# Kernel optimization log

Hardware: AMD Instinct MI355X
Metric: run time of the kernel (lower is better)

Reference implementation:

```python
import jax, jax.numpy as jnp
import numpy as np

X_SIZE = 1024
N_HEADS = 16
N_BASIS = 10
MAX_LEN = 4096
CACHE_KEEP_LEN = 4096
B = 8
T_NEW = 128
T_PREV = 4096
HEAD_DIM = X_SIZE // N_HEADS
LN_EPS = 1e-5


def setup_inputs() -> dict:
    key = jax.random.key(0)
    ks = jax.random.split(key, 9)
    def w(k, shape, s):
        return jax.random.normal(k, shape, dtype=jnp.float32) * s
    inv = 1.0 / np.sqrt(X_SIZE)
    return {
        "X": w(ks[0], (B, T_NEW, X_SIZE), 1.0),
        "cache_K": w(ks[1], (B, T_PREV, X_SIZE), 1.0),
        "cache_V": w(ks[2], (B, T_PREV, X_SIZE), 1.0),
        "Wq": w(ks[3], (X_SIZE, X_SIZE), 0.1 * inv),   # Q_SCALE=0.1 (NormedLinear init scale)
        "bq": jnp.zeros((X_SIZE,), jnp.float32),
        "Wk": w(ks[4], (X_SIZE, X_SIZE), 0.2 * inv),   # K_SCALE=0.2, no bias
        "Wv": w(ks[5], (X_SIZE, X_SIZE), 1.0 * inv),   # V_SCALE*sqrt(scale), no bias
        "Wproj": w(ks[6], (X_SIZE, X_SIZE), 1.0 * inv),
        "bproj": jnp.zeros((X_SIZE,), jnp.float32),
        "Wr": w(ks[7], (X_SIZE, N_BASIS * N_HEADS), 0.1 * inv),  # R_SCALE=0.1
        "br": jnp.zeros((N_BASIS * N_HEADS,), jnp.float32),
        "b_nd": w(ks[8], (N_BASIS, MAX_LEN), 0.2),     # B_SCALE=0.2
        "ln_g": jnp.ones((X_SIZE,), jnp.float32),
        "ln_b": jnp.zeros((X_SIZE,), jnp.float32),
    }


def _split_heads(x, h):
    b, t, e = x.shape
    return x.reshape(b, t, h, e // h).transpose(0, 2, 1, 3).reshape(b * h, t, e // h)


def _merge_heads(x, h):
    bh, t, q = x.shape
    b = bh // h
    return x.reshape(b, h, t, q).transpose(0, 2, 1, 3).reshape(b, t, h * q)


def reference(X, cache_K, cache_V, Wq, bq, Wk, Wv, Wproj, bproj, Wr, br, b_nd, ln_g, ln_b):
    Bsz, t, E = X.shape
    # ln_x
    mu = jnp.mean(X, axis=-1, keepdims=True)
    var = jnp.var(X, axis=-1, keepdims=True)
    Xn = (X - mu) / jnp.sqrt(var + LN_EPS) * ln_g + ln_b
    # projections on new tokens
    Q = Xn @ Wq + bq
    K_new = Xn @ Wk
    V_new = Xn @ Wv
    # update_state: append cache (startfull=max(Tprev-cache_keep_len,0))
    Tprev = cache_K.shape[1]
    start = max(Tprev - CACHE_KEEP_LEN, 0)
    Kf = jnp.concatenate([cache_K[:, start:], K_new], axis=1)  # (B, T, E)
    Vf = jnp.concatenate([cache_V[:, start:], V_new], axis=1)
    T = Kf.shape[1]
    Qh = _split_heads(Q, N_HEADS)   # (B*h, t, q)
    Kh = _split_heads(Kf, N_HEADS)  # (B*h, T, q)
    Vh = _split_heads(Vf, N_HEADS)
    # relattn logits: R_btn (B*h, t, n_basis), bandified basis D_ntT
    R = _split_heads(Xn @ Wr + br, N_HEADS)
    d = (T - t + jnp.arange(t)[:, None]) - jnp.arange(T)[None, :]  # (t, T) time diff
    valid = (d >= 0) & (d < MAX_LEN)
    D = jnp.where(valid[None, :, :], b_nd[:, jnp.clip(d, 0, MAX_LEN - 1)], 0.0)  # (n, t, T)
    extra = jnp.einsum('btn,ntT->btT', R, D)  # (B*h, t, T)
    # causal band bias (mask=None -> default causal mask with maxlen window)
    bias = jnp.where(valid, 0.0, -1e9)[None, :, :]
    logits = bias + extra + jnp.einsum('btq,bTq->btT', Qh, Kh) * (1.0 / np.sqrt(HEAD_DIM))
    W_btT = jax.nn.softmax(logits, axis=-1)
    A = _merge_heads(jnp.einsum('btT,bTq->btq', W_btT, Vh), N_HEADS)  # (B, t, E)
    return X + (A @ Wproj + bproj)
```

## Files before the change

kernel.cpp:

```cpp
#include <hip/hip_runtime.h>
#include <hip/hip_bf16.h>

typedef __bf16 bf16;
typedef __bf16 bf16x8 __attribute__((ext_vector_type(8)));
typedef float f32x4 __attribute__((ext_vector_type(4)));
typedef unsigned short u16;
typedef u16 u16x4 __attribute__((ext_vector_type(4)));

#define MFMA16(a, b, c) __builtin_amdgcn_mfma_f32_16x16x32_bf16(a, b, c, 0, 0, 0)
#define LOG2E 1.44269504f

static __device__ __forceinline__ bf16x8 cvt8(float4 a, float4 b) {
  union { bf16 h[8]; bf16x8 v; } u;
  u.h[0] = (bf16)a.x; u.h[1] = (bf16)a.y; u.h[2] = (bf16)a.z; u.h[3] = (bf16)a.w;
  u.h[4] = (bf16)b.x; u.h[5] = (bf16)b.y; u.h[6] = (bf16)b.z; u.h[7] = (bf16)b.w;
  return u.v;
}

__global__ __launch_bounds__(256) void k_ln(const float* __restrict__ X,
                                            const float* __restrict__ g,
                                            const float* __restrict__ bb,
                                            bf16* __restrict__ Xn) {
  int m = blockIdx.x, t = threadIdx.x;
  const float* row = X + (size_t)m * 1024;
  float4 x = ((const float4*)row)[t];
  float s1 = x.x + x.y + x.z + x.w;
  float s2 = x.x * x.x + x.y * x.y + x.z * x.z + x.w * x.w;
#pragma unroll
  for (int off = 1; off < 64; off <<= 1) {
    s1 += __shfl_xor(s1, off);
    s2 += __shfl_xor(s2, off);
  }
  __shared__ float ws1[4], ws2[4];
  int w = t >> 6;
  if ((t & 63) == 0) { ws1[w] = s1; ws2[w] = s2; }
  __syncthreads();
  s1 = ws1[0] + ws1[1] + ws1[2] + ws1[3];
  s2 = ws2[0] + ws2[1] + ws2[2] + ws2[3];
  float mu = s1 * (1.f / 1024.f);
  float var = s2 * (1.f / 1024.f) - mu * mu;
  float rstd = rsqrtf(var + 1e-5f);
  float4 gg = ((const float4*)g)[t];
  float4 bv = ((const float4*)bb)[t];
  union { bf16 h[4]; u16x4 v; } u;
  u.h[0] = (bf16)((x.x - mu) * rstd * gg.x + bv.x);
  u.h[1] = (bf16)((x.y - mu) * rstd * gg.y + bv.y);
  u.h[2] = (bf16)((x.z - mu) * rstd * gg.z + bv.z);
  u.h[3] = (bf16)((x.w - mu) * rstd * gg.w + bv.w);
  ((u16x4*)(Xn + (size_t)m * 1024))[t] = u.v;
}

__global__ __launch_bounds__(256) void k_convert(const float* __restrict__ Wq,
                                                 const float* __restrict__ Wk,
                                                 const float* __restrict__ Wv,
                                                 const float* __restrict__ Wr,
                                                 const float* __restrict__ Wp,
                                                 bf16* __restrict__ Wt_all,
                                                 bf16* __restrict__ Wpt) {
  __shared__ float tile[64][65];
  int t = threadIdx.x;
  int bn = blockIdx.x / 16, bk = blockIdx.x % 16;
  int n0 = bn * 64, k0 = bk * 64;
#pragma unroll
  for (int it = 0; it < 16; ++it) {
    int idx = t + 256 * it;
    int kl = idx >> 6, nl = idx & 63;
    int n = n0 + nl, k = k0 + kl;
    float v;
    if (n < 1024)       v = Wq[(size_t)k * 1024 + n];
    else if (n < 2048)  v = Wk[(size_t)k * 1024 + (n - 1024)];
    else if (n < 3072)  v = Wv[(size_t)k * 1024 + (n - 2048)];
    else if (n < 3232)  v = Wr[(size_t)k * 160 + (n - 3072)];
    else if (n < 3328)  v = 0.f;
    else                v = Wp[(size_t)k * 1024 + (n - 3328)];
    tile[kl][nl] = v;
  }
  __syncthreads();
#pragma unroll
  for (int it = 0; it < 16; ++it) {
    int idx = t + 256 * it;
    int nl = idx >> 6, kl = idx & 63;
    int n = n0 + nl, k = k0 + kl;
    bf16 v = (bf16)tile[kl][nl];
    if (n < 3328) Wt_all[(size_t)n * 1024 + k] = v;
    else          Wpt[(size_t)(n - 3328) * 1024 + k] = v;
  }
}

template <int MODE>
__global__ __launch_bounds__(256) void k_gemm(const bf16* __restrict__ A,
                                              const bf16* __restrict__ Bw,
                                              bf16* __restrict__ Qb, bf16* __restrict__ Kn,
                                              bf16* __restrict__ Vn, float* __restrict__ Rws,
                                              const float* __restrict__ bq,
                                              const float* __restrict__ br,
                                              float* __restrict__ Out,
                                              const float* __restrict__ bproj,
                                              const float* __restrict__ Xres) {
  __shared__ __align__(16) bf16 As[128][72];
  __shared__ __align__(16) bf16 Bs[128][72];
  int t = threadIdx.x, l = t & 63, wid = t >> 6;
  int ln = l & 15, grp = l >> 4;
  int m0 = blockIdx.y * 128, n0 = blockIdx.x * 128;
  int wr = wid >> 1, wc = wid & 1;
  f32x4 acc[4][4] = {};
  int srow = t >> 1, shalf = (t & 1) * 32;

  for (int kt = 0; kt < 16; ++kt) {
    int k0 = kt * 64;
    const bf16* asrc = A + (size_t)(m0 + srow) * 1024 + k0 + shalf;
    const bf16* bsrc = Bw + (size_t)(n0 + srow) * 1024 + k0 + shalf;
    bf16x8 a0 = ((const bf16x8*)asrc)[0], a1 = ((const bf16x8*)asrc)[1];
    bf16x8 a2 = ((const bf16x8*)asrc)[2], a3 = ((const bf16x8*)asrc)[3];
    bf16x8 b0 = ((const bf16x8*)bsrc)[0], b1 = ((const bf16x8*)bsrc)[1];
    bf16x8 b2 = ((const bf16x8*)bsrc)[2], b3 = ((const bf16x8*)bsrc)[3];
    __syncthreads();
    *(bf16x8*)&As[srow][shalf + 0] = a0;  *(bf16x8*)&As[srow][shalf + 8] = a1;
    *(bf16x8*)&As[srow][shalf + 16] = a2; *(bf16x8*)&As[srow][shalf + 24] = a3;
    *(bf16x8*)&Bs[srow][shalf + 0] = b0;  *(bf16x8*)&Bs[srow][shalf + 8] = b1;
    *(bf16x8*)&Bs[srow][shalf + 16] = b2; *(bf16x8*)&Bs[srow][shalf + 24] = b3;
    __syncthreads();
#pragma unroll
    for (int ks = 0; ks < 2; ++ks) {
      int kk = ks * 32 + grp * 8;
      bf16x8 af[4], bf[4];
#pragma unroll
      for (int is = 0; is < 4; ++is) af[is] = *(const bf16x8*)&As[wr * 64 + is * 16 + ln][kk];
#pragma unroll
      for (int js = 0; js < 4; ++js) bf[js] = *(const bf16x8*)&Bs[wc * 64 + js * 16 + ln][kk];
#pragma unroll
      for (int is = 0; is < 4; ++is)
#pragma unroll
        for (int js = 0; js < 4; ++js) acc[is][js] = MFMA16(af[is], bf[js], acc[is][js]);
    }
  }

#pragma unroll
  for (int is = 0; is < 4; ++is)
#pragma unroll
    for (int js = 0; js < 4; ++js)
#pragma unroll
      for (int r = 0; r < 4; ++r) {
        int m = m0 + wr * 64 + is * 16 + grp * 4 + r;
        int n = n0 + wc * 64 + js * 16 + ln;
        float v = acc[is][js][r];
        if (MODE == 0) {
          int b = m >> 7, il = m & 127;
          if (n < 1024) {
            int h = n >> 6, dm = n & 63;
            Qb[((size_t)(b * 16 + h) * 128 + il) * 64 + dm] = (bf16)((v + bq[n]) * (0.125f * LOG2E));
          } else if (n < 2048) {
            Kn[(size_t)m * 1024 + (n - 1024)] = (bf16)v;
          } else if (n < 3072) {
            Vn[(size_t)m * 1024 + (n - 2048)] = (bf16)v;
          } else if (n < 3232) {
            int e = n - 3072, hh = e / 10, nb = e - hh * 10;
            Rws[((size_t)(b * 16 + hh) * 128 + il) * 10 + nb] = v + br[e];
          }
        } else {
          Out[(size_t)m * 1024 + n] = v + bproj[n] + Xres[(size_t)m * 1024 + n];
        }
      }
}

__global__ __launch_bounds__(512, 4) void k_attn(const float* __restrict__ cacheK,
                                                 const float* __restrict__ cacheV,
                                                 const bf16* __restrict__ Kn,
                                                 const bf16* __restrict__ Vn,
                                                 const bf16* __restrict__ Qb,
                                                 const float* __restrict__ Rws,
                                                 const float* __restrict__ bnd,
                                                 bf16* __restrict__ Opart,
                                                 float* __restrict__ mws,
                                                 float* __restrict__ lws) {
  __shared__ __align__(16) bf16 Ks[2][32][72];
  __shared__ __align__(16) bf16 Vt[2][64][36];
  __shared__ __align__(16) bf16 Gw[8][48][20];
  __shared__ __align__(16) bf16 bTf[516][16];

  int t = threadIdx.x, l = t & 63, w = t >> 6;
  int grp = l >> 4, ln = l & 15;
  int s = blockIdx.x % 12, bh = blockIdx.x / 12;
  int b = bh >> 4, h = bh & 15;
  int jbase = s * 352;
  int dlo0 = 4033 - jbase;

  {
    int q = t;
    int d = dlo0 - 320 + q;
    d = d < 0 ? 0 : (d > 4095 ? 4095 : d);
#pragma unroll
    for (int n = 0; n < 10; ++n) bTf[q][n] = (bf16)bnd[(size_t)n * 4096 + d];
#pragma unroll
    for (int n = 10; n < 16; ++n) bTf[q][n] = (bf16)0.f;
  }
  if (t < 4) {
#pragma unroll
    for (int n = 0; n < 16; ++n) bTf[512 + t][n] = (bf16)0.f;
  }

  int iq = w * 16 + ln;
  bf16x8 qf[2];
  qf[0] = *(const bf16x8*)(Qb + ((size_t)bh * 128 + iq) * 64 + grp * 8);
  qf[1] = *(const bf16x8*)(Qb + ((size_t)bh * 128 + iq) * 64 + 32 + grp * 8);
  bf16x8 rf;
  {
    union { bf16 hh[8]; bf16x8 v; } u;
    const float* rrow = Rws + ((size_t)bh * 128 + iq) * 10;
#pragma unroll
    for (int e = 0; e < 8; ++e) {
      int k = grp * 8 + e;
      u.hh[e] = (bf16)(k < 10 ? rrow[k] * LOG2E : 0.f);
    }
    rf = u.v;
  }

  int krow = t >> 4, kcb = (t & 15) * 4;
  int vjl = t & 31, vd0 = (t >> 5) * 4;
  int vsp = (((vjl >> 2) & 3) << 3) | (((vjl >> 4) & 1) << 2) | (vjl & 3);

  float4 kA, vA;

  auto issue = [&](int jt0) {
    if (jt0 < 4096) {
      kA = *(const float4*)(cacheK + ((size_t)(b * 4096 + jt0 + krow)) * 1024 + h * 64 + kcb);
      vA = *(const float4*)(cacheV + ((size_t)(b * 4096 + jt0 + vjl)) * 1024 + h * 64 + vd0);
    } else {
      u16x4 kN = *(const u16x4*)(Kn + ((size_t)(b * 128 + (jt0 + krow - 4096))) * 1024 + h * 64 + kcb);
      u16x4 vN = *(const u16x4*)(Vn + ((size_t)(b * 128 + (jt0 + vjl - 4096))) * 1024 + h * 64 + vd0);
      union { u16 u; bf16 h; } c;
      c.u = kN[0]; kA.x = (float)c.h; c.u = kN[1]; kA.y = (float)c.h;
      c.u = kN[2]; kA.z = (float)c.h; c.u = kN[3]; kA.w = (float)c.h;
      c.u = vN[0]; vA.x = (float)c.h; c.u = vN[1]; vA.y = (float)c.h;
      c.u = vN[2]; vA.z = (float)c.h; c.u = vN[3]; vA.w = (float)c.h;
    }
  };
  auto stage = [&](int p) {
    union { bf16 hh[4]; u16x4 v; } ku;
    ku.hh[0] = (bf16)kA.x; ku.hh[1] = (bf16)kA.y;
    ku.hh[2] = (bf16)kA.z; ku.hh[3] = (bf16)kA.w;
    *(u16x4*)&Ks[p][krow][kcb] = ku.v;
    Vt[p][vd0 + 0][vsp] = (bf16)vA.x; Vt[p][vd0 + 1][vsp] = (bf16)vA.y;
    Vt[p][vd0 + 2][vsp] = (bf16)vA.z; Vt[p][vd0 + 3][vsp] = (bf16)vA.w;
  };

  issue(jbase);
  stage(0);
  issue(jbase + 32);

  f32x4 Oacc[4] = {};
  float m_r = -1e30f, l_r = 0.f;

  for (int tt = 0; tt < 11; ++tt) {
    int jt0 = jbase + tt * 32;
    int cur = tt & 1;
    __syncthreads();
    if (tt + 1 < 11) stage(cur ^ 1);
    if (tt + 2 < 11) issue(jbase + (tt + 2) * 32);

    __builtin_amdgcn_s_setprio(1);
    f32x4 Sacc[2] = {};
#pragma unroll
    for (int ks = 0; ks < 2; ++ks) {
      int kk = ks * 32 + grp * 8;
#pragma unroll
      for (int js = 0; js < 2; ++js) {
        bf16x8 bfr = *(const bf16x8*)&Ks[cur][js * 16 + ln][kk];
        Sacc[js] = MFMA16(bfr, qf[ks], Sacc[js]);
      }
    }
    int qb = 352 - 32 * tt;
#pragma unroll
    for (int u = 0; u < 3; ++u) {
      bf16x8 bfr = *(const bf16x8*)&bTf[qb + w * 16 + u * 16 + ln][grp * 8];
      f32x4 z = {};
      f32x4 g = MFMA16(rf, bfr, z);
      union { bf16 hh[4]; u16x4 v; } uu;
      uu.hh[0] = (bf16)g[0]; uu.hh[1] = (bf16)g[1];
      uu.hh[2] = (bf16)g[2]; uu.hh[3] = (bf16)g[3];
      *(u16x4*)&Gw[w][u * 16 + ln][grp * 4] = uu.v;
    }
    __builtin_amdgcn_s_setprio(0);

    float mx = -1e30f;
    if (jt0 >= 128 && jt0 < 4066) {
#pragma unroll
      for (int js = 0; js < 2; ++js)
#pragma unroll
        for (int r = 0; r < 4; ++r) {
          int jj = js * 16 + grp * 4 + r;
          int cl = ln - jj + 31;
          float v = Sacc[js][r] + (float)Gw[w][cl][ln];
          Sacc[js][r] = v;
          mx = fmaxf(mx, v);
        }
    } else {
#pragma unroll
      for (int js = 0; js < 2; ++js)
#pragma unroll
        for (int r = 0; r < 4; ++r) {
          int jj = js * 16 + grp * 4 + r;
          int d = 4096 + iq - (jt0 + jj);
          bool valid = ((unsigned)d) < 4096u;
          int cl = ln - jj + 31;
          float g = (float)Gw[w][cl][ln];
          float v = valid ? (Sacc[js][r] + g) : -1e9f;
          Sacc[js][r] = v;
          mx = fmaxf(mx, v);
        }
    }
    mx = fmaxf(mx, __shfl_xor(mx, 16));
    mx = fmaxf(mx, __shfl_xor(mx, 32));

    if (!__all(mx <= m_r + 8.f)) {
      float mnew = fmaxf(m_r, mx);
      float scn = exp2f(m_r - mnew);
      m_r = mnew;
      l_r *= scn;
#pragma unroll
      for (int r = 0; r < 4; ++r) {
        float scr = __shfl(scn, grp * 4 + r, 16);
#pragma unroll
        for (int ds = 0; ds < 4; ++ds) Oacc[ds][r] *= scr;
      }
    }

    union { bf16 hh[8]; bf16x8 v; } p0;
    float rsl = 0.f;
#pragma unroll
    for (int js = 0; js < 2; ++js)
#pragma unroll
      for (int r = 0; r < 4; ++r) {
        float p = exp2f(Sacc[js][r] - m_r);
        rsl += p;
        p0.hh[js * 4 + r] = (bf16)p;
      }
    l_r += rsl;

    __builtin_amdgcn_s_setprio(1);
#pragma unroll
    for (int ds = 0; ds < 4; ++ds) {
      bf16x8 v0 = *(const bf16x8*)&Vt[cur][ds * 16 + ln][grp * 8];
      Oacc[ds] = MFMA16(p0.v, v0, Oacc[ds]);
    }
    __builtin_amdgcn_s_setprio(0);
  }

  l_r += __shfl_xor(l_r, 16);
  l_r += __shfl_xor(l_r, 32);

  int part = s * 128 + bh;
#pragma unroll
  for (int ds = 0; ds < 4; ++ds)
#pragma unroll
    for (int r = 0; r < 4; ++r) {
      int il = w * 16 + grp * 4 + r;
      Opart[((size_t)part * 128 + il) * 64 + ds * 16 + ln] = (bf16)Oacc[ds][r];
    }
  if (grp == 0) {
    mws[(size_t)part * 128 + iq] = m_r;
    lws[(size_t)part * 128 + iq] = l_r;
  }
}

__global__ __launch_bounds__(256) void k_combine(const bf16* __restrict__ Opart,
                                                 const float* __restrict__ mws,
                                                 const float* __restrict__ lws,
                                                 bf16* __restrict__ Aout) {
  __shared__ float msh[12][32], lsh[12][32];
  int bh = blockIdx.x, q = blockIdx.y, t = threadIdx.x;
  int b = bh >> 4, h = bh & 15;
  for (int idx = t; idx < 384; idx += 256) {
    int s = idx >> 5, io = idx & 31;
    msh[s][io] = mws[(size_t)(s * 128 + bh) * 128 + q * 32 + io];
    lsh[s][io] = lws[(size_t)(s * 128 + bh) * 128 + q * 32 + io];
  }
  __syncthreads();
  int dm = t & 63, i4 = t >> 6;
  for (int ii = 0; ii < 8; ++ii) {
    int io = i4 * 8 + ii;
    int i = q * 32 + io;
    float M = -1e30f;
#pragma unroll
    for (int s = 0; s < 12; ++s) M = fmaxf(M, msh[s][io]);
    float L = 0.f, acc = 0.f;
#pragma unroll
    for (int s = 0; s < 12; ++s) {
      float wgt = exp2f(msh[s][io] - M);
      L += wgt * lsh[s][io];
      acc += wgt * (float)Opart[((size_t)(s * 128 + bh) * 128 + i) * 64 + dm];
    }
    Aout[((size_t)(b * 128 + i)) * 1024 + h * 64 + dm] = (bf16)(acc / L);
  }
}

extern "C" void kernel_launch(void* const* d_in, const int* in_sizes, int n_in,
                              void* d_out, int out_size, void* d_ws, size_t ws_size,
                              hipStream_t stream) {
  (void)in_sizes; (void)n_in; (void)out_size; (void)ws_size;
  const float* X      = (const float*)d_in[0];
  const float* cacheK = (const float*)d_in[1];
  const float* cacheV = (const float*)d_in[2];
  const float* Wq     = (const float*)d_in[3];
  const float* bq     = (const float*)d_in[4];
  const float* Wk     = (const float*)d_in[5];
  const float* Wv     = (const float*)d_in[6];
  const float* Wproj  = (const float*)d_in[7];
  const float* bproj  = (const float*)d_in[8];
  const float* Wr     = (const float*)d_in[9];
  const float* br     = (const float*)d_in[10];
  const float* bnd    = (const float*)d_in[11];
  const float* lng    = (const float*)d_in[12];
  const float* lnb    = (const float*)d_in[13];
  float* out = (float*)d_out;

  char* ws = (char*)d_ws;
  bf16* Wt_all = (bf16*)ws;  ws += (size_t)3328 * 1024 * 2;
  bf16* Wpt    = (bf16*)ws;  ws += (size_t)1024 * 1024 * 2;
  bf16* Xn     = (bf16*)ws;  ws += (size_t)1024 * 1024 * 2;
  bf16* Qb     = (bf16*)ws;  ws += (size_t)1024 * 1024 * 2;
  bf16* Kn     = (bf16*)ws;  ws += (size_t)1024 * 1024 * 2;
  bf16* Vn     = (bf16*)ws;  ws += (size_t)1024 * 1024 * 2;
  bf16* Aattn  = (bf16*)ws;  ws += (size_t)1024 * 1024 * 2;
  float* Rws   = (float*)ws; ws += (size_t)128 * 128 * 10 * 4;
  float* mws   = (float*)ws; ws += (size_t)12 * 128 * 128 * 4;
  float* lws   = (float*)ws; ws += (size_t)12 * 128 * 128 * 4;
  bf16* Opart  = (bf16*)ws;  ws += (size_t)12 * 128 * 128 * 64 * 2;

  k_convert<<<dim3(68 * 16), 256, 0, stream>>>(Wq, Wk, Wv, Wr, Wproj, Wt_all, Wpt);
  k_ln<<<dim3(1024), 256, 0, stream>>>(X, lng, lnb, Xn);
  k_gemm<0><<<dim3(26, 8), 256, 0, stream>>>(Xn, Wt_all, Qb, Kn, Vn, Rws, bq, br,
                                             nullptr, nullptr, nullptr);
  k_attn<<<dim3(1536), 512, 0, stream>>>(cacheK, cacheV, Kn, Vn, Qb, Rws, bnd,
                                         Opart, mws, lws);
  k_combine<<<dim3(128, 4), 256, 0, stream>>>(Opart, mws, lws, Aattn);
  k_gemm<1><<<dim3(8, 8), 256, 0, stream>>>(Aattn, Wpt, nullptr, nullptr, nullptr,
                                            nullptr, nullptr, nullptr, out, bproj, X);
}
```

Before: 163.1 us.

## Halve attention block size with two query sub-tiles per wave

Each attention block now runs 4 waves of 256 threads instead of 8 waves of 512, and each wave handles 32 queries as two 16-row sub-tiles. K and V fragments read from LDS are reused across both sub-tiles. Global K/V staging also moves to 8-element loads per thread. The goal is fewer LDS reads and less softmax bookkeeping per MFMA. The cost is more registers and fewer resident waves to hide the latency of the fp32 cache loads.

```diff
diff --git a/kernel.cpp b/kernel.cpp
--- a/kernel.cpp
+++ b/kernel.cpp
@@ -163,7 +163,7 @@
       }
 }
 
-__global__ __launch_bounds__(512, 4) void k_attn(const float* __restrict__ cacheK,
+__global__ __launch_bounds__(256, 3) void k_attn(const float* __restrict__ cacheK,
                                                  const float* __restrict__ cacheV,
                                                  const bf16* __restrict__ Kn,
                                                  const bf16* __restrict__ Vn,
@@ -175,8 +175,8 @@
                                                  float* __restrict__ lws) {
   __shared__ __align__(16) bf16 Ks[2][32][72];
   __shared__ __align__(16) bf16 Vt[2][64][36];
-  __shared__ __align__(16) bf16 Gw[8][48][20];
-  __shared__ __align__(16) bf16 bTf[516][16];
+  __shared__ __align__(16) bf16 Gw[4][64][36];
+  __shared__ __align__(16) bf16 bTf[480][16];
 
   int t = threadIdx.x, l = t & 63, w = t >> 6;
   int grp = l >> 4, ln = l & 15;
@@ -185,71 +185,70 @@
   int jbase = s * 352;
   int dlo0 = 4033 - jbase;
 
-  {
-    int q = t;
-    int d = dlo0 - 320 + q;
+  for (int q = t; q < 480; q += 256) {
+    int d = dlo0 - 288 + q;
     d = d < 0 ? 0 : (d > 4095 ? 4095 : d);
 #pragma unroll
     for (int n = 0; n < 10; ++n) bTf[q][n] = (bf16)bnd[(size_t)n * 4096 + d];
 #pragma unroll
     for (int n = 10; n < 16; ++n) bTf[q][n] = (bf16)0.f;
   }
-  if (t < 4) {
-#pragma unroll
-    for (int n = 0; n < 16; ++n) bTf[512 + t][n] = (bf16)0.f;
-  }
-
-  int iq = w * 16 + ln;
-  bf16x8 qf[2];
-  qf[0] = *(const bf16x8*)(Qb + ((size_t)bh * 128 + iq) * 64 + grp * 8);
-  qf[1] = *(const bf16x8*)(Qb + ((size_t)bh * 128 + iq) * 64 + 32 + grp * 8);
-  bf16x8 rf;
-  {
-    union { bf16 hh[8]; bf16x8 v; } u;
-    const float* rrow = Rws + ((size_t)bh * 128 + iq) * 10;
+
+  int iqb = w * 32 + ln;
+  bf16x8 qf[2][2];
+  bf16x8 rf[2];
+#pragma unroll
+  for (int hh = 0; hh < 2; ++hh) {
+    const bf16* qrow = Qb + ((size_t)bh * 128 + iqb + hh * 16) * 64;
+    qf[hh][0] = *(const bf16x8*)(qrow + grp * 8);
+    qf[hh][1] = *(const bf16x8*)(qrow + 32 + grp * 8);
+    union { bf16 x[8]; bf16x8 v; } u;
+    const float* rrow = Rws + ((size_t)bh * 128 + iqb + hh * 16) * 10;
 #pragma unroll
     for (int e = 0; e < 8; ++e) {
       int k = grp * 8 + e;
-      u.hh[e] = (bf16)(k < 10 ? rrow[k] * LOG2E : 0.f);
-    }
-    rf = u.v;
-  }
-
-  int krow = t >> 4, kcb = (t & 15) * 4;
-  int vjl = t & 31, vd0 = (t >> 5) * 4;
+      u.x[e] = (bf16)(k < 10 ? rrow[k] * LOG2E : 0.f);
+    }
+    rf[hh] = u.v;
+  }
+
+  int krow = t >> 3, kcb = (t & 7) * 8;
+  int vjl = t & 31, vd0 = (t >> 5) * 8;
   int vsp = (((vjl >> 2) & 3) << 3) | (((vjl >> 4) & 1) << 2) | (vjl & 3);
 
-  float4 kA, vA;
+  float4 kA, kB, vA, vB;
 
   auto issue = [&](int jt0) {
     if (jt0 < 4096) {
-      kA = *(const float4*)(cacheK + ((size_t)(b * 4096 + jt0 + krow)) * 1024 + h * 64 + kcb);
-      vA = *(const float4*)(cacheV + ((size_t)(b * 4096 + jt0 + vjl)) * 1024 + h * 64 + vd0);
+      const float* sk = cacheK + ((size_t)(b * 4096 + jt0 + krow)) * 1024 + h * 64 + kcb;
+      kA = *(const float4*)sk;
+      kB = *(const float4*)(sk + 4);
+      const float* sv = cacheV + ((size_t)(b * 4096 + jt0 + vjl)) * 1024 + h * 64 + vd0;
+      vA = *(const float4*)sv;
+      vB = *(const float4*)(sv + 4);
     } else {
-      u16x4 kN = *(const u16x4*)(Kn + ((size_t)(b * 128 + (jt0 + krow - 4096))) * 1024 + h * 64 + kcb);
-      u16x4 vN = *(const u16x4*)(Vn + ((size_t)(b * 128 + (jt0 + vjl - 4096))) * 1024 + h * 64 + vd0);
-      union { u16 u; bf16 h; } c;
-      c.u = kN[0]; kA.x = (float)c.h; c.u = kN[1]; kA.y = (float)c.h;
-      c.u = kN[2]; kA.z = (float)c.h; c.u = kN[3]; kA.w = (float)c.h;
-      c.u = vN[0]; vA.x = (float)c.h; c.u = vN[1]; vA.y = (float)c.h;
-      c.u = vN[2]; vA.z = (float)c.h; c.u = vN[3]; vA.w = (float)c.h;
+      bf16x8 kN = *(const bf16x8*)(Kn + ((size_t)(b * 128 + (jt0 + krow - 4096))) * 1024 + h * 64 + kcb);
+      bf16x8 vN = *(const bf16x8*)(Vn + ((size_t)(b * 128 + (jt0 + vjl - 4096))) * 1024 + h * 64 + vd0);
+      kA = make_float4((float)kN[0], (float)kN[1], (float)kN[2], (float)kN[3]);
+      kB = make_float4((float)kN[4], (float)kN[5], (float)kN[6], (float)kN[7]);
+      vA = make_float4((float)vN[0], (float)vN[1], (float)vN[2], (float)vN[3]);
+      vB = make_float4((float)vN[4], (float)vN[5], (float)vN[6], (float)vN[7]);
     }
   };
   auto stage = [&](int p) {
-    union { bf16 hh[4]; u16x4 v; } ku;
-    ku.hh[0] = (bf16)kA.x; ku.hh[1] = (bf16)kA.y;
-    ku.hh[2] = (bf16)kA.z; ku.hh[3] = (bf16)kA.w;
-    *(u16x4*)&Ks[p][krow][kcb] = ku.v;
+    *(bf16x8*)&Ks[p][krow][kcb] = cvt8(kA, kB);
     Vt[p][vd0 + 0][vsp] = (bf16)vA.x; Vt[p][vd0 + 1][vsp] = (bf16)vA.y;
     Vt[p][vd0 + 2][vsp] = (bf16)vA.z; Vt[p][vd0 + 3][vsp] = (bf16)vA.w;
+    Vt[p][vd0 + 4][vsp] = (bf16)vB.x; Vt[p][vd0 + 5][vsp] = (bf16)vB.y;
+    Vt[p][vd0 + 6][vsp] = (bf16)vB.z; Vt[p][vd0 + 7][vsp] = (bf16)vB.w;
   };
 
   issue(jbase);
   stage(0);
   issue(jbase + 32);
 
-  f32x4 Oacc[4] = {};
-  float m_r = -1e30f, l_r = 0.f;
+  f32x4 Oacc[2][4] = {};
+  float m_r[2] = {-1e30f, -1e30f}, l_r[2] = {0.f, 0.f};
 
   for (int tt = 0; tt < 11; ++tt) {
     int jt0 = jbase + tt * 32;
@@ -258,108 +257,142 @@
     if (tt + 1 < 11) stage(cur ^ 1);
     if (tt + 2 < 11) issue(jbase + (tt + 2) * 32);
 
+    bf16x8 kf[2][2];
+#pragma unroll
+    for (int js = 0; js < 2; ++js)
+#pragma unroll
+      for (int ks = 0; ks < 2; ++ks)
+        kf[js][ks] = *(const bf16x8*)&Ks[cur][js * 16 + ln][ks * 32 + grp * 8];
+
     __builtin_amdgcn_s_setprio(1);
-    f32x4 Sacc[2] = {};
-#pragma unroll
-    for (int ks = 0; ks < 2; ++ks) {
-      int kk = ks * 32 + grp * 8;
-#pragma unroll
-      for (int js = 0; js < 2; ++js) {
-        bf16x8 bfr = *(const bf16x8*)&Ks[cur][js * 16 + ln][kk];
-        Sacc[js] = MFMA16(bfr, qf[ks], Sacc[js]);
+    f32x4 Sacc[2][2] = {};
+#pragma unroll
+    for (int hh = 0; hh < 2; ++hh)
+#pragma unroll
+      for (int ks = 0; ks < 2; ++ks)
+#pragma unroll
+        for (int js = 0; js < 2; ++js)
+          Sacc[hh][js] = MFMA16(kf[js][ks], qf[hh][ks], Sacc[hh][js]);
+
+    int qb = 320 - 32 * tt + w * 32;
+#pragma unroll
+    for (int hh = 0; hh < 2; ++hh)
+#pragma unroll
+      for (int u = 0; u < 3; ++u) {
+        bf16x8 bfr = *(const bf16x8*)&bTf[qb + hh * 16 + u * 16 + ln][grp * 8];
+        f32x4 z = {};
+        f32x4 g = MFMA16(rf[hh], bfr, z);
+        union { bf16 x[4]; u16x4 v; } uu;
+        uu.x[0] = (bf16)g[0]; uu.x[1] = (bf16)g[1];
+        uu.x[2] = (bf16)g[2]; uu.x[3] = (bf16)g[3];
+        *(u16x4*)&Gw[w][hh * 16 + u * 16 + ln][hh * 16 + grp * 4] = uu.v;
       }
-    }
-    int qb = 352 - 32 * tt;
-#pragma unroll
-    for (int u = 0; u < 3; ++u) {
-      bf16x8 bfr = *(const bf16x8*)&bTf[qb + w * 16 + u * 16 + ln][grp * 8];
-      f32x4 z = {};
-      f32x4 g = MFMA16(rf, bfr, z);
-      union { bf16 hh[4]; u16x4 v; } uu;
-      uu.hh[0] = (bf16)g[0]; uu.hh[1] = (bf16)g[1];
-      uu.hh[2] = (bf16)g[2]; uu.hh[3] = (bf16)g[3];
-      *(u16x4*)&Gw[w][u * 16 + ln][grp * 4] = uu.v;
-    }
     __builtin_amdgcn_s_setprio(0);
 
-    float mx = -1e30f;
+    float mx[2] = {-1e30f, -1e30f};
     if (jt0 >= 128 && jt0 < 4066) {
 #pragma unroll
+      for (int hh = 0; hh < 2; ++hh)
+#pragma unroll
+        for (int js = 0; js < 2; ++js)
+#pragma unroll
+          for (int r = 0; r < 4; ++r) {
+            int jj = js * 16 + grp * 4 + r;
+            int cl = hh * 16 + ln - jj + 31;
+            float v = Sacc[hh][js][r] + (float)Gw[w][cl][hh * 16 + ln];
+            Sacc[hh][js][r] = v;
+            mx[hh] = fmaxf(mx[hh], v);
+          }
+    } else {
+#pragma unroll
+      for (int hh = 0; hh < 2; ++hh)
+#pragma unroll
+        for (int js = 0; js < 2; ++js)
+#pragma unroll
+          for (int r = 0; r < 4; ++r) {
+            int jj = js * 16 + grp * 4 + r;
+            int iq = iqb + hh * 16;
+            int d = 4096 + iq - (jt0 + jj);
+            bool valid = ((unsigned)d) < 4096u;
+            int cl = hh * 16 + ln - jj + 31;
+            float g = (float)Gw[w][cl][hh * 16 + ln];
+            float v = valid ? (Sacc[hh][js][r] + g) : -1e9f;
+            Sacc[hh][js][r] = v;
+            mx[hh] = fmaxf(mx[hh], v);
+          }
+    }
+#pragma unroll
+    for (int hh = 0; hh < 2; ++hh) {
+      mx[hh] = fmaxf(mx[hh], __shfl_xor(mx[hh], 16));
+      mx[hh] = fmaxf(mx[hh], __shfl_xor(mx[hh], 32));
+    }
+
+    bool ok = (mx[0] <= m_r[0] + 8.f) && (mx[1] <= m_r[1] + 8.f);
+    if (!__all(ok)) {
+#pragma unroll
+      for (int hh = 0; hh < 2; ++hh) {
+        float mnew = fmaxf(m_r[hh], mx[hh]);
+        float scn = exp2f(m_r[hh] - mnew);
+        m_r[hh] = mnew;
+        l_r[hh] *= scn;
+#pragma unroll
+        for (int r = 0; r < 4; ++r) {
+          float scr = __shfl(scn, grp * 4 + r, 16);
+#pragma unroll
+          for (int ds = 0; ds < 4; ++ds) Oacc[hh][ds][r] *= scr;
+        }
+      }
+    }
+
+    union { bf16 x[8]; bf16x8 v; } p[2];
+#pragma unroll
+    for (int hh = 0; hh < 2; ++hh) {
+      float rsl = 0.f;
+#pragma unroll
       for (int js = 0; js < 2; ++js)
 #pragma unroll
         for (int r = 0; r < 4; ++r) {
-          int jj = js * 16 + grp * 4 + r;
-          int cl = ln - jj + 31;
-          float v = Sacc[js][r] + (float)Gw[w][cl][ln];
-          Sacc[js][r] = v;
-          mx = fmaxf(mx, v);
+          float pv = exp2f(Sacc[hh][js][r] - m_r[hh]);
+          rsl += pv;
+          p[hh].x[js * 4 + r] = (bf16)pv;
         }
-    } else {
-#pragma unroll
-      for (int js = 0; js < 2; ++js)
-#pragma unroll
-        for (int r = 0; r < 4; ++r) {
-          int jj = js * 16 + grp * 4 + r;
-          int d = 4096 + iq - (jt0 + jj);
-          bool valid = ((unsigned)d) < 4096u;
-          int cl = ln - jj + 31;
-          float g = (float)Gw[w][cl][ln];
-          float v = valid ? (Sacc[js][r] + g) : -1e9f;
-          Sacc[js][r] = v;
-          mx = fmaxf(mx, v);
-        }
-    }
-    mx = fmaxf(mx, __shfl_xor(mx, 16));
-    mx = fmaxf(mx, __shfl_xor(mx, 32));
-
-    if (!__all(mx <= m_r + 8.f)) {
-      float mnew = fmaxf(m_r, mx);
-      float scn = exp2f(m_r - mnew);
-      m_r = mnew;
-      l_r *= scn;
+      l_r[hh] += rsl;
+    }
+    bf16x8 vf[4];
+#pragma unroll
+    for (int ds = 0; ds < 4; ++ds) vf[ds] = *(const bf16x8*)&Vt[cur][ds * 16 + ln][grp * 8];
+
+    __builtin_amdgcn_s_setprio(1);
+#pragma unroll
+    for (int hh = 0; hh < 2; ++hh)
+#pragma unroll
+      for (int ds = 0; ds < 4; ++ds)
+        Oacc[hh][ds] = MFMA16(p[hh].v, vf[ds], Oacc[hh][ds]);
+    __builtin_amdgcn_s_setprio(0);
+  }
+
+#pragma unroll
+  for (int hh = 0; hh < 2; ++hh) {
+    l_r[hh] += __shfl_xor(l_r[hh], 16);
+    l_r[hh] += __shfl_xor(l_r[hh], 32);
+  }
+
+  int part = s * 128 + bh;
+#pragma unroll
+  for (int hh = 0; hh < 2; ++hh)
+#pragma unroll
+    for (int ds = 0; ds < 4; ++ds)
 #pragma unroll
       for (int r = 0; r < 4; ++r) {
-        float scr = __shfl(scn, grp * 4 + r, 16);
-#pragma unroll
-        for (int ds = 0; ds < 4; ++ds) Oacc[ds][r] *= scr;
+        int il = w * 32 + hh * 16 + grp * 4 + r;
+        Opart[((size_t)part * 128 + il) * 64 + ds * 16 + ln] = (bf16)Oacc[hh][ds][r];
       }
-    }
-
-    union { bf16 hh[8]; bf16x8 v; } p0;
-    float rsl = 0.f;
-#pragma unroll
-    for (int js = 0; js < 2; ++js)
-#pragma unroll
-      for (int r = 0; r < 4; ++r) {
-        float p = exp2f(Sacc[js][r] - m_r);
-        rsl += p;
-        p0.hh[js * 4 + r] = (bf16)p;
-      }
-    l_r += rsl;
-
-    __builtin_amdgcn_s_setprio(1);
-#pragma unroll
-    for (int ds = 0; ds < 4; ++ds) {
-      bf16x8 v0 = *(const bf16x8*)&Vt[cur][ds * 16 + ln][grp * 8];
-      Oacc[ds] = MFMA16(p0.v, v0, Oacc[ds]);
-    }
-    __builtin_amdgcn_s_setprio(0);
-  }
-
-  l_r += __shfl_xor(l_r, 16);
-  l_r += __shfl_xor(l_r, 32);
-
-  int part = s * 128 + bh;
-#pragma unroll
-  for (int ds = 0; ds < 4; ++ds)
-#pragma unroll
-    for (int r = 0; r < 4; ++r) {
-      int il = w * 16 + grp * 4 + r;
-      Opart[((size_t)part * 128 + il) * 64 + ds * 16 + ln] = (bf16)Oacc[ds][r];
-    }
   if (grp == 0) {
-    mws[(size_t)part * 128 + iq] = m_r;
-    lws[(size_t)part * 128 + iq] = l_r;
+#pragma unroll
+    for (int hh = 0; hh < 2; ++hh) {
+      mws[(size_t)part * 128 + iqb + hh * 16] = m_r[hh];
+      lws[(size_t)part * 128 + iqb + hh * 16] = l_r[hh];
+    }
   }
 }
 
@@ -431,7 +464,7 @@
   k_ln<<<dim3(1024), 256, 0, stream>>>(X, lng, lnb, Xn);
   k_gemm<0><<<dim3(26, 8), 256, 0, stream>>>(Xn, Wt_all, Qb, Kn, Vn, Rws, bq, br,
                                              nullptr, nullptr, nullptr);
-  k_attn<<<dim3(1536), 512, 0, stream>>>(cacheK, cacheV, Kn, Vn, Qb, Rws, bnd,
+  k_attn<<<dim3(1536), 256, 0, stream>>>(cacheK, cacheV, Kn, Vn, Qb, Rws, bnd,
                                          Opart, mws, lws);
   k_combine<<<dim3(128, 4), 256, 0, stream>>>(Opart, mws, lws, Aattn);
   k_gemm<1><<<dim3(8, 8), 256, 0, stream>>>(Aattn, Wpt, nullptr, nullptr, nullptr,
```

Result: slower. 166.8 us (+2.3%).

## Halve attention key splits and restage relative-basis table mid-loop

Applied to the files above, without the earlier changes.

Cuts the split-K count of the attention kernel from 12 to 6, so each block walks 704 keys in 22 tiles instead of 352 in 11. The relative-basis table is restaged halfway through the loop, behind an extra barrier. The table row width also shrinks from 16 to 12 bf16, with fragments read as two 8-byte loads. This halves the partial-output writes and the combine reads, but leaves fewer blocks (768) to fill the GPU and lengthens each block's serial loop.

```diff
diff --git a/kernel.cpp b/kernel.cpp
--- a/kernel.cpp
+++ b/kernel.cpp
@@ -176,28 +176,30 @@
   __shared__ __align__(16) bf16 Ks[2][32][72];
   __shared__ __align__(16) bf16 Vt[2][64][36];
   __shared__ __align__(16) bf16 Gw[8][48][20];
-  __shared__ __align__(16) bf16 bTf[516][16];
+  __shared__ __align__(16) bf16 bTf[516][12];
 
   int t = threadIdx.x, l = t & 63, w = t >> 6;
   int grp = l >> 4, ln = l & 15;
-  int s = blockIdx.x % 12, bh = blockIdx.x / 12;
+  int s = blockIdx.x % 6, bh = blockIdx.x / 6;
   int b = bh >> 4, h = bh & 15;
-  int jbase = s * 352;
+  int jbase = s * 704;
   int dlo0 = 4033 - jbase;
 
-  {
-    int q = t;
-    int d = dlo0 - 320 + q;
-    d = d < 0 ? 0 : (d > 4095 ? 4095 : d);
-#pragma unroll
-    for (int n = 0; n < 10; ++n) bTf[q][n] = (bf16)bnd[(size_t)n * 4096 + d];
-#pragma unroll
-    for (int n = 10; n < 16; ++n) bTf[q][n] = (bf16)0.f;
-  }
-  if (t < 4) {
-#pragma unroll
-    for (int n = 0; n < 16; ++n) bTf[512 + t][n] = (bf16)0.f;
-  }
+  auto stage_bT = [&](int hf) {
+    if (t < 512) {
+      int q = t;
+      int d = dlo0 - 352 * hf - 320 + q;
+      d = d < 0 ? 0 : (d > 4095 ? 4095 : d);
+#pragma unroll
+      for (int n = 0; n < 10; ++n) bTf[q][n] = (bf16)bnd[(size_t)n * 4096 + d];
+      bTf[q][10] = (bf16)0.f; bTf[q][11] = (bf16)0.f;
+    }
+    if (t < 4) {
+#pragma unroll
+      for (int n = 0; n < 12; ++n) bTf[512 + t][n] = (bf16)0.f;
+    }
+  };
+  stage_bT(0);
 
   int iq = w * 16 + ln;
   bf16x8 qf[2];
@@ -251,12 +253,18 @@
   f32x4 Oacc[4] = {};
   float m_r = -1e30f, l_r = 0.f;
 
-  for (int tt = 0; tt < 11; ++tt) {
+  for (int tt = 0; tt < 22; ++tt) {
     int jt0 = jbase + tt * 32;
     int cur = tt & 1;
     __syncthreads();
-    if (tt + 1 < 11) stage(cur ^ 1);
-    if (tt + 2 < 11) issue(jbase + (tt + 2) * 32);
+    if (tt == 11) {
+      stage_bT(1);
+      __syncthreads();
+    }
+    if (tt + 1 < 22) stage(cur ^ 1);
+    if (tt + 2 < 22) issue(jbase + (tt + 2) * 32);
+
+    int ttl = tt < 11 ? tt : tt - 11;
 
     __builtin_amdgcn_s_setprio(1);
     f32x4 Sacc[2] = {};
@@ -269,16 +277,20 @@
         Sacc[js] = MFMA16(bfr, qf[ks], Sacc[js]);
       }
     }
-    int qb = 352 - 32 * tt;
+    int qb = 352 - 32 * ttl + w * 16;
 #pragma unroll
     for (int u = 0; u < 3; ++u) {
-      bf16x8 bfr = *(const bf16x8*)&bTf[qb + w * 16 + u * 16 + ln][grp * 8];
+      int row = qb + u * 16 + ln;
+      const u16* src = (const u16*)bTf + row * 12 + grp * 8;
+      union { uint2 q2[2]; bf16x8 v; } bu;
+      bu.q2[0] = *(const uint2*)src;
+      bu.q2[1] = *(const uint2*)(src + 4);
       f32x4 z = {};
-      f32x4 g = MFMA16(rf, bfr, z);
-      union { bf16 hh[4]; u16x4 v; } uu;
+      f32x4 g = MFMA16(rf, bu.v, z);
+      union { bf16 hh[4]; u16x4 v4; } uu;
       uu.hh[0] = (bf16)g[0]; uu.hh[1] = (bf16)g[1];
       uu.hh[2] = (bf16)g[2]; uu.hh[3] = (bf16)g[3];
-      *(u16x4*)&Gw[w][u * 16 + ln][grp * 4] = uu.v;
+      *(u16x4*)&Gw[w][u * 16 + ln][grp * 4] = uu.v4;
     }
     __builtin_amdgcn_s_setprio(0);
 
@@ -367,11 +379,11 @@
                                                  const float* __restrict__ mws,
                                                  const float* __restrict__ lws,
                                                  bf16* __restrict__ Aout) {
-  __shared__ float msh[12][32], lsh[12][32];
+  __shared__ float msh[6][32], lsh[6][32];
   int bh = blockIdx.x, q = blockIdx.y, t = threadIdx.x;
   int b = bh >> 4, h = bh & 15;
-  for (int idx = t; idx < 384; idx += 256) {
-    int s = idx >> 5, io = idx & 31;
+  if (t < 192) {
+    int s = t >> 5, io = t & 31;
     msh[s][io] = mws[(size_t)(s * 128 + bh) * 128 + q * 32 + io];
     lsh[s][io] = lws[(size_t)(s * 128 + bh) * 128 + q * 32 + io];
   }
@@ -382,10 +394,10 @@
     int i = q * 32 + io;
     float M = -1e30f;
 #pragma unroll
-    for (int s = 0; s < 12; ++s) M = fmaxf(M, msh[s][io]);
+    for (int s = 0; s < 6; ++s) M = fmaxf(M, msh[s][io]);
     float L = 0.f, acc = 0.f;
 #pragma unroll
-    for (int s = 0; s < 12; ++s) {
+    for (int s = 0; s < 6; ++s) {
       float wgt = exp2f(msh[s][io] - M);
       L += wgt * lsh[s][io];
       acc += wgt * (float)Opart[((size_t)(s * 128 + bh) * 128 + i) * 64 + dm];
@@ -423,16 +435,16 @@
   bf16* Vn     = (bf16*)ws;  ws += (size_t)1024 * 1024 * 2;
   bf16* Aattn  = (bf16*)ws;  ws += (size_t)1024 * 1024 * 2;
   float* Rws   = (float*)ws; ws += (size_t)128 * 128 * 10 * 4;
-  float* mws   = (float*)ws; ws += (size_t)12 * 128 * 128 * 4;
-  float* lws   = (float*)ws; ws += (size_t)12 * 128 * 128 * 4;
-  bf16* Opart  = (bf16*)ws;  ws += (size_t)12 * 128 * 128 * 64 * 2;
+  float* mws   = (float*)ws; ws += (size_t)6 * 128 * 128 * 4;
+  float* lws   = (float*)ws; ws += (size_t)6 * 128 * 128 * 4;
+  bf16* Opart  = (bf16*)ws;  ws += (size_t)6 * 128 * 128 * 64 * 2;
 
   k_convert<<<dim3(68 * 16), 256, 0, stream>>>(Wq, Wk, Wv, Wr, Wproj, Wt_all, Wpt);
   k_ln<<<dim3(1024), 256, 0, stream>>>(X, lng, lnb, Xn);
   k_gemm<0><<<dim3(26, 8), 256, 0, stream>>>(Xn, Wt_all, Qb, Kn, Vn, Rws, bq, br,
                                              nullptr, nullptr, nullptr);
-  k_attn<<<dim3(1536), 512, 0, stream>>>(cacheK, cacheV, Kn, Vn, Qb, Rws, bnd,
-                                         Opart, mws, lws);
+  k_attn<<<dim3(768), 512, 0, stream>>>(cacheK, cacheV, Kn, Vn, Qb, Rws, bnd,
+                                        Opart, mws, lws);
   k_combine<<<dim3(128, 4), 256, 0, stream>>>(Opart, mws, lws, Aattn);
   k_gemm<1><<<dim3(8, 8), 256, 0, stream>>>(Aattn, Wpt, nullptr, nullptr, nullptr,
                                             nullptr, nullptr, nullptr, out, bproj, X);
```

Measured after the change: 171.7 us. +5.3%, slower.

## Split attention blocks into two query halves with 256 threads each

Applied to the files above, without the earlier changes.

The attention kernel now launches twice as many 256-thread blocks, each handling 64 of the 128 query rows for a (batch, head, key-split) triple. Each thread stages 8 K/V elements per tile instead of 4, and the relative-basis LDS table is narrowed from 16 to 12 columns and read with two 8-byte loads. The aim is finer-grained scheduling and less LDS per block, giving more resident blocks. The cost is that each K/V tile is now fetched from global memory by two blocks, which relies on the paired adjacent blocks sharing cache.

```diff
diff --git a/kernel.cpp b/kernel.cpp
--- a/kernel.cpp
+++ b/kernel.cpp
@@ -163,7 +163,7 @@
       }
 }
 
-__global__ __launch_bounds__(512, 4) void k_attn(const float* __restrict__ cacheK,
+__global__ __launch_bounds__(256, 4) void k_attn(const float* __restrict__ cacheK,
                                                  const float* __restrict__ cacheV,
                                                  const bf16* __restrict__ Kn,
                                                  const bf16* __restrict__ Vn,
@@ -175,31 +175,34 @@
                                                  float* __restrict__ lws) {
   __shared__ __align__(16) bf16 Ks[2][32][72];
   __shared__ __align__(16) bf16 Vt[2][64][36];
-  __shared__ __align__(16) bf16 Gw[8][48][20];
-  __shared__ __align__(16) bf16 bTf[516][16];
+  __shared__ __align__(16) bf16 Gw[4][48][20];
+  __shared__ __align__(16) bf16 bTf[516][12];
 
   int t = threadIdx.x, l = t & 63, w = t >> 6;
   int grp = l >> 4, ln = l & 15;
-  int s = blockIdx.x % 12, bh = blockIdx.x / 12;
+  int bid = blockIdx.x;
+  int qh = bid & 1;
+  int s = (bid >> 1) % 12;
+  int bh = bid / 24;
   int b = bh >> 4, h = bh & 15;
   int jbase = s * 352;
   int dlo0 = 4033 - jbase;
-
-  {
-    int q = t;
-    int d = dlo0 - 320 + q;
-    d = d < 0 ? 0 : (d > 4095 ? 4095 : d);
-#pragma unroll
-    for (int n = 0; n < 10; ++n) bTf[q][n] = (bf16)bnd[(size_t)n * 4096 + d];
-#pragma unroll
-    for (int n = 10; n < 16; ++n) bTf[q][n] = (bf16)0.f;
-  }
-  if (t < 4) {
-#pragma unroll
-    for (int n = 0; n < 16; ++n) bTf[512 + t][n] = (bf16)0.f;
-  }
-
-  int iq = w * 16 + ln;
+  int qoff = qh * 64;
+
+  for (int q = t; q < 516; q += 256) {
+    if (q < 512) {
+      int d = dlo0 - 320 + q;
+      d = d < 0 ? 0 : (d > 4095 ? 4095 : d);
+#pragma unroll
+      for (int n = 0; n < 10; ++n) bTf[q][n] = (bf16)bnd[(size_t)n * 4096 + d];
+      bTf[q][10] = (bf16)0.f; bTf[q][11] = (bf16)0.f;
+    } else {
+#pragma unroll
+      for (int n = 0; n < 12; ++n) bTf[q][n] = (bf16)0.f;
+    }
+  }
+
+  int iq = qoff + w * 16 + ln;
   bf16x8 qf[2];
   qf[0] = *(const bf16x8*)(Qb + ((size_t)bh * 128 + iq) * 64 + grp * 8);
   qf[1] = *(const bf16x8*)(Qb + ((size_t)bh * 128 + iq) * 64 + 32 + grp * 8);
@@ -215,33 +218,35 @@
     rf = u.v;
   }
 
-  int krow = t >> 4, kcb = (t & 15) * 4;
-  int vjl = t & 31, vd0 = (t >> 5) * 4;
+  int krow = t >> 3, kcb = (t & 7) * 8;
+  int vjl = t & 31, vd0 = (t >> 5) * 8;
   int vsp = (((vjl >> 2) & 3) << 3) | (((vjl >> 4) & 1) << 2) | (vjl & 3);
 
-  float4 kA, vA;
+  float4 kA, kB, vA, vB;
 
   auto issue = [&](int jt0) {
     if (jt0 < 4096) {
-      kA = *(const float4*)(cacheK + ((size_t)(b * 4096 + jt0 + krow)) * 1024 + h * 64 + kcb);
-      vA = *(const float4*)(cacheV + ((size_t)(b * 4096 + jt0 + vjl)) * 1024 + h * 64 + vd0);
+      const float* sk = cacheK + ((size_t)(b * 4096 + jt0 + krow)) * 1024 + h * 64 + kcb;
+      kA = *(const float4*)sk;
+      kB = *(const float4*)(sk + 4);
+      const float* sv = cacheV + ((size_t)(b * 4096 + jt0 + vjl)) * 1024 + h * 64 + vd0;
+      vA = *(const float4*)sv;
+      vB = *(const float4*)(sv + 4);
     } else {
-      u16x4 kN = *(const u16x4*)(Kn + ((size_t)(b * 128 + (jt0 + krow - 4096))) * 1024 + h * 64 + kcb);
-      u16x4 vN = *(const u16x4*)(Vn + ((size_t)(b * 128 + (jt0 + vjl - 4096))) * 1024 + h * 64 + vd0);
-      union { u16 u; bf16 h; } c;
-      c.u = kN[0]; kA.x = (float)c.h; c.u = kN[1]; kA.y = (float)c.h;
-      c.u = kN[2]; kA.z = (float)c.h; c.u = kN[3]; kA.w = (float)c.h;
-      c.u = vN[0]; vA.x = (float)c.h; c.u = vN[1]; vA.y = (float)c.h;
-      c.u = vN[2]; vA.z = (float)c.h; c.u = vN[3]; vA.w = (float)c.h;
+      bf16x8 kN = *(const bf16x8*)(Kn + ((size_t)(b * 128 + (jt0 + krow - 4096))) * 1024 + h * 64 + kcb);
+      bf16x8 vN = *(const bf16x8*)(Vn + ((size_t)(b * 128 + (jt0 + vjl - 4096))) * 1024 + h * 64 + vd0);
+      kA = make_float4((float)kN[0], (float)kN[1], (float)kN[2], (float)kN[3]);
+      kB = make_float4((float)kN[4], (float)kN[5], (float)kN[6], (float)kN[7]);
+      vA = make_float4((float)vN[0], (float)vN[1], (float)vN[2], (float)vN[3]);
+      vB = make_float4((float)vN[4], (float)vN[5], (float)vN[6], (float)vN[7]);
     }
   };
   auto stage = [&](int p) {
-    union { bf16 hh[4]; u16x4 v; } ku;
-    ku.hh[0] = (bf16)kA.x; ku.hh[1] = (bf16)kA.y;
-    ku.hh[2] = (bf16)kA.z; ku.hh[3] = (bf16)kA.w;
-    *(u16x4*)&Ks[p][krow][kcb] = ku.v;
+    *(bf16x8*)&Ks[p][krow][kcb] = cvt8(kA, kB);
     Vt[p][vd0 + 0][vsp] = (bf16)vA.x; Vt[p][vd0 + 1][vsp] = (bf16)vA.y;
     Vt[p][vd0 + 2][vsp] = (bf16)vA.z; Vt[p][vd0 + 3][vsp] = (bf16)vA.w;
+    Vt[p][vd0 + 4][vsp] = (bf16)vB.x; Vt[p][vd0 + 5][vsp] = (bf16)vB.y;
+    Vt[p][vd0 + 6][vsp] = (bf16)vB.z; Vt[p][vd0 + 7][vsp] = (bf16)vB.w;
   };
 
   issue(jbase);
@@ -269,21 +274,26 @@
         Sacc[js] = MFMA16(bfr, qf[ks], Sacc[js]);
       }
     }
-    int qb = 352 - 32 * tt;
+    int qb = 352 - 32 * tt + qoff + w * 16;
 #pragma unroll
     for (int u = 0; u < 3; ++u) {
-      bf16x8 bfr = *(const bf16x8*)&bTf[qb + w * 16 + u * 16 + ln][grp * 8];
+      int row = qb + u * 16 + ln;
+      const u16* src = (const u16*)bTf + row * 12 + grp * 8;
+      union { uint2 q2[2]; bf16x8 v; } bu;
+      bu.q2[0] = *(const uint2*)src;
+      bu.q2[1] = *(const uint2*)(src + 4);
       f32x4 z = {};
-      f32x4 g = MFMA16(rf, bfr, z);
-      union { bf16 hh[4]; u16x4 v; } uu;
+      f32x4 g = MFMA16(rf, bu.v, z);
+      union { bf16 hh[4]; u16x4 v4; } uu;
       uu.hh[0] = (bf16)g[0]; uu.hh[1] = (bf16)g[1];
       uu.hh[2] = (bf16)g[2]; uu.hh[3] = (bf16)g[3];
-      *(u16x4*)&Gw[w][u * 16 + ln][grp * 4] = uu.v;
+      *(u16x4*)&Gw[w][u * 16 + ln][grp * 4] = uu.v4;
     }
     __builtin_amdgcn_s_setprio(0);
 
     float mx = -1e30f;
-    if (jt0 >= 128 && jt0 < 4066) {
+    int jadj = jt0 - qoff;
+    if (jadj >= 64 && jadj < 4066) {
 #pragma unroll
       for (int js = 0; js < 2; ++js)
 #pragma unroll
@@ -354,7 +364,7 @@
   for (int ds = 0; ds < 4; ++ds)
 #pragma unroll
     for (int r = 0; r < 4; ++r) {
-      int il = w * 16 + grp * 4 + r;
+      int il = qoff + w * 16 + grp * 4 + r;
       Opart[((size_t)part * 128 + il) * 64 + ds * 16 + ln] = (bf16)Oacc[ds][r];
     }
   if (grp == 0) {
@@ -431,7 +441,7 @@
   k_ln<<<dim3(1024), 256, 0, stream>>>(X, lng, lnb, Xn);
   k_gemm<0><<<dim3(26, 8), 256, 0, stream>>>(Xn, Wt_all, Qb, Kn, Vn, Rws, bq, br,
                                              nullptr, nullptr, nullptr);
-  k_attn<<<dim3(1536), 512, 0, stream>>>(cacheK, cacheV, Kn, Vn, Qb, Rws, bnd,
+  k_attn<<<dim3(3072), 256, 0, stream>>>(cacheK, cacheV, Kn, Vn, Qb, Rws, bnd,
                                          Opart, mws, lws);
   k_combine<<<dim3(128, 4), 256, 0, stream>>>(Opart, mws, lws, Aattn);
   k_gemm<1><<<dim3(8, 8), 256, 0, stream>>>(Aattn, Wpt, nullptr, nullptr, nullptr,
```

After: 192.1 us. 17.8% more time.
